# Kernel optimization log

Measured on AMD Instinct MI355X. Metric: run time of the kernel, lower is better.

## Reference

```python
import jax, jax.numpy as jnp
import numpy as np

B, N, D = 16, 128, 128

def setup_inputs() -> dict:
    key = jax.random.key(0)
    ks = jax.random.split(key, 7)
    h = jax.random.normal(ks[0], (B, N, D), dtype=jnp.float32)
    adj = jax.random.randint(ks[1], (B, N, N), 0, 2).astype(jnp.float32)
    e = jax.random.normal(ks[2], (B, N, N, D), dtype=jnp.float32)
    # torch.nn.Linear weights: [out_features, in_features]
    Wm = jax.random.normal(ks[3], (D, 3 * D), dtype=jnp.float32) * (1.0 / np.sqrt(3 * D))
    bm = jax.random.normal(ks[4], (D,), dtype=jnp.float32) * 0.01
    Wu = jax.random.normal(ks[5], (D, 2 * D), dtype=jnp.float32) * (1.0 / np.sqrt(2 * D))
    bu = jax.random.normal(ks[6], (D,), dtype=jnp.float32) * 0.01
    return {"h": h, "adj": adj, "e": e, "Wm": Wm, "bm": bm, "Wu": Wu, "bu": bu}

def reference(h, adj, e, Wm, bm, Wu, bu):
    # Split the message Linear over the concat [h_i, h_j, e] -> three matmuls
    # (same math as cat+Linear, without materializing the [B,N,N,3D] tensor).
    d = h.shape[-1]
    W1, W2, W3 = Wm[:, :d], Wm[:, d:2 * d], Wm[:, 2 * d:]
    hi = jnp.einsum('bnd,kd->bnk', h, W1)            # sender term  [B,N,Dout]
    hj = jnp.einsum('bnd,kd->bnk', h, W2)            # receiver term [B,N,Dout]
    me = jnp.einsum('bijd,kd->bijk', e, W3)          # edge term     [B,N,N,Dout]
    m = hi[:, :, None, :] + hj[:, None, :, :] + me + bm  # [B,N,N,Dout]
    m = m * adj[..., None]                            # mask by adjacency
    m = m.sum(axis=1)                                 # sum over senders i -> [B,N,Dout]
    h_cat = jnp.concatenate([h, m], axis=2)           # [B,N,2D]
    return jnp.einsum('bnd,kd->bnk', h_cat, Wu) + bu  # [B,N,D]
```

## Files before the change

### kernel.cpp

```cpp
#include <hip/hip_runtime.h>
#include <hip/hip_bf16.h>

#define BB 16
#define NN 128
#define DD 128

typedef __attribute__((ext_vector_type(8))) short s8v;
typedef __attribute__((ext_vector_type(4))) float f4v;

__device__ __forceinline__ unsigned short f2bf(float f) {
    __hip_bfloat16 b = __float2bfloat16(f);
    return *reinterpret_cast<unsigned short*>(&b);
}

__global__ __launch_bounds__(256) void prep_kernel(
    const float* __restrict__ h, const float* __restrict__ Wm,
    const float* __restrict__ bm, const float* __restrict__ Wu,
    unsigned short* __restrict__ BT, float* __restrict__ bmWu,
    unsigned short* __restrict__ hbf) {
    const int g = blockIdx.x, t = threadIdx.x;
    if (g < 48) {
        __shared__ float WuB_s[128][129];
        for (int p = 0; p < 64; ++p) {
            const int x = p * 256 + t;
            WuB_s[x & 127][x >> 7] = Wu[(x >> 7) * 256 + 128 + (x & 127)];
        }
        __syncthreads();
        const int m = g >> 4, dc = g & 15;
        const int off   = (m == 0) ? 0   : (m == 1) ? 256 : 128;
        const int rbase = (m == 0) ? 128 : (m == 1) ? 256 : 384;
        const int k = t & 127, dh = t >> 7;
        const int d0 = dc * 8 + dh * 4;
        float a0 = 0, a1 = 0, a2 = 0, a3 = 0;
        for (int kk = 0; kk < 128; ++kk) {
            const float wu = WuB_s[kk][k];
            const float* wmp = Wm + kk * 384 + off + d0;
            a0 += wmp[0] * wu; a1 += wmp[1] * wu;
            a2 += wmp[2] * wu; a3 += wmp[3] * wu;
        }
        unsigned short* bp = BT + (size_t)k * 512 + rbase + d0;
        bp[0] = f2bf(a0); bp[1] = f2bf(a1); bp[2] = f2bf(a2); bp[3] = f2bf(a3);
    } else if (g == 48) {
        for (int p = 0; p < 64; ++p) {
            const int x = p * 256 + t, k = x >> 7, d = x & 127;
            BT[(size_t)k * 512 + d] = f2bf(Wu[k * 256 + d]);
        }
        if (t < 128) {
            float s = 0.f;
            for (int kk = 0; kk < 128; ++kk) s += bm[kk] * Wu[t * 256 + 128 + kk];
            bmWu[t] = s;
        }
    } else {
        const int bi = g - 49;
        const float4* h4 = (const float4*)h;
        uint2* hb2 = (uint2*)hbf;
        for (int p = 0; p < 32; ++p) {
            const int i4 = bi * 8192 + p * 256 + t;
            const float4 v = h4[i4];
            hb2[i4] = make_uint2((unsigned)f2bf(v.x) | ((unsigned)f2bf(v.y) << 16),
                                 (unsigned)f2bf(v.z) | ((unsigned)f2bf(v.w) << 16));
        }
    }
}

__global__ __launch_bounds__(256) void es_kernel(const float* __restrict__ e,
                                                 const float* __restrict__ adj,
                                                 unsigned short* __restrict__ esbf) {
    const int bj = blockIdx.x, t = threadIdx.x;
    const int b = bj >> 7, j = bj & 127;
    __shared__ float adj_s[NN];
    __shared__ float4 red[8][32];
    if (t < NN) adj_s[t] = adj[(size_t)(b * NN + t) * NN + j];
    __syncthreads();
    const int d4 = t & 31, ig = t >> 5;
    const float4* __restrict__ e4 =
        (const float4*)e + ((size_t)(b * NN) * NN + j) * 32 + d4;
    const int i0 = ig * 16;
    float4 acc = make_float4(0.f, 0.f, 0.f, 0.f);
    #pragma unroll
    for (int ii = 0; ii < 16; ++ii) {
        const float a = adj_s[i0 + ii];
        if (a != 0.0f) {
            const float4 v = e4[(size_t)(i0 + ii) * (NN * 32)];
            acc.x += a * v.x; acc.y += a * v.y;
            acc.z += a * v.z; acc.w += a * v.w;
        }
    }
    red[ig][d4] = acc;
    __syncthreads();
    if (t < 32) {
        float4 s = red[0][t];
        #pragma unroll
        for (int r = 1; r < 8; ++r) {
            const float4 v = red[r][t];
            s.x += v.x; s.y += v.y; s.z += v.z; s.w += v.w;
        }
        ((uint2*)esbf)[(size_t)bj * 32 + t] =
            make_uint2((unsigned)f2bf(s.x) | ((unsigned)f2bf(s.y) << 16),
                       (unsigned)f2bf(s.z) | ((unsigned)f2bf(s.w) << 16));
    }
}

__global__ __launch_bounds__(1024) void ah_kernel(
    const float* __restrict__ h, const float* __restrict__ adj,
    unsigned short* __restrict__ AHbf, float* __restrict__ deg) {
    const int blk = blockIdx.x;
    const int b = blk >> 4, jbase = (blk & 15) * 8;
    const int t = threadIdx.x;
    __shared__ float adj_s[8][NN];
    {
        const int i = t >> 3, j2 = t & 7;
        adj_s[j2][i] = adj[(size_t)(b * NN + i) * NN + jbase + j2];
    }
    __syncthreads();
    if (t < 256) {
        const int jj = t >> 5, l = t & 31;
        float s = adj_s[jj][l] + adj_s[jj][l + 32] + adj_s[jj][l + 64] + adj_s[jj][l + 96];
        #pragma unroll
        for (int off = 16; off; off >>= 1) s += __shfl_xor(s, off);
        if (l == 0) deg[b * NN + jbase + jj] = s;
    }
    const int k = t & 127, jl = t >> 7;
    float a0 = 0.f;
    const float* __restrict__ hp = h + (size_t)b * NN * DD + k;
    #pragma unroll 8
    for (int m = 0; m < 32; ++m) {
        const float4 aA = *(const float4*)&adj_s[jl][4 * m];
        const float h0 = hp[(size_t)(4 * m + 0) * DD];
        const float h1 = hp[(size_t)(4 * m + 1) * DD];
        const float h2 = hp[(size_t)(4 * m + 2) * DD];
        const float h3 = hp[(size_t)(4 * m + 3) * DD];
        a0 += aA.x * h0 + aA.y * h1 + aA.z * h2 + aA.w * h3;
    }
    AHbf[(size_t)(b * NN + jbase + jl) * DD + k] = f2bf(a0);
}

__global__ __launch_bounds__(256) void out_kernel(
    const unsigned short* __restrict__ hbf, const unsigned short* __restrict__ AHbf,
    const unsigned short* __restrict__ esbf, const unsigned short* __restrict__ BT,
    const float* __restrict__ deg, const float* __restrict__ bmWu,
    const float* __restrict__ bu, float* __restrict__ out) {
    const int rt = blockIdx.x >> 2, ct = blockIdx.x & 3;
    const int t = threadIdx.x;
    const int l = t & 63, wid = t >> 6, mw = wid >> 1, nw = wid & 1;
    __shared__ unsigned short A_s[32][72], B_s[32][72], B2_s[32][72];
    f4v acc1 = {0.f, 0.f, 0.f, 0.f};
    f4v acc2 = {0.f, 0.f, 0.f, 0.f};
    const int rA = t >> 3, cb = t & 7;
    const int arow = mw * 16 + (l & 15);
    const int brow = nw * 16 + (l & 15);
    const int lg = l >> 4;
    for (int c = 0; c < 6; ++c) {
        __syncthreads();
        const unsigned short* src = (c < 2) ? hbf : (c < 4) ? AHbf : esbf;
        const int col0 = (c & 1) * 64;
        const int rowg = rt * 32 + rA;
        *(s8v*)&A_s[rA][cb * 8] = *(const s8v*)&src[(size_t)rowg * 128 + col0 + cb * 8];
        *(s8v*)&B_s[rA][cb * 8] =
            *(const s8v*)&BT[(size_t)(ct * 32 + rA) * 512 + c * 64 + cb * 8];
        if (c < 2)
            *(s8v*)&B2_s[rA][cb * 8] =
                *(const s8v*)&BT[(size_t)(ct * 32 + rA) * 512 + 384 + c * 64 + cb * 8];
        __syncthreads();
        #pragma unroll
        for (int kit = 0; kit < 2; ++kit) {
            const s8v a  = *(const s8v*)&A_s[arow][kit * 32 + lg * 8];
            const s8v bb = *(const s8v*)&B_s[brow][kit * 32 + lg * 8];
            acc1 = __builtin_amdgcn_mfma_f32_16x16x32_bf16(a, bb, acc1, 0, 0, 0);
            if (c < 2) {
                const s8v b2 = *(const s8v*)&B2_s[brow][kit * 32 + lg * 8];
                acc2 = __builtin_amdgcn_mfma_f32_16x16x32_bf16(a, b2, acc2, 0, 0, 0);
            }
        }
    }
    const int colk = ct * 32 + nw * 16 + (l & 15);
    const float bmv = bmWu[colk], buv = bu[colk];
    #pragma unroll
    for (int r = 0; r < 4; ++r) {
        const int rowg = rt * 32 + mw * 16 + (l >> 4) * 4 + r;
        const float dg = deg[rowg];
        out[(size_t)rowg * 128 + colk] = acc1[r] + dg * acc2[r] + dg * bmv + buv;
    }
}

extern "C" void kernel_launch(void* const* d_in, const int* in_sizes, int n_in,
                              void* d_out, int out_size, void* d_ws, size_t ws_size,
                              hipStream_t stream) {
    const float* h   = (const float*)d_in[0];
    const float* adj = (const float*)d_in[1];
    const float* e   = (const float*)d_in[2];
    const float* Wm  = (const float*)d_in[3];
    const float* bm  = (const float*)d_in[4];
    const float* Wu  = (const float*)d_in[5];
    const float* bu  = (const float*)d_in[6];
    float* out = (float*)d_out;

    float* ws = (float*)d_ws;
    unsigned short* BT   = (unsigned short*)ws;
    float*          bmWu = ws + 32768;
    float*          deg  = ws + 32896;
    unsigned short* hbf  = (unsigned short*)(ws + 34944);
    unsigned short* AHbf = (unsigned short*)(ws + 166016);
    unsigned short* esbf = (unsigned short*)(ws + 297088);

    prep_kernel<<<57, 256, 0, stream>>>(h, Wm, bm, Wu, BT, bmWu, hbf);
    es_kernel<<<BB * NN, 256, 0, stream>>>(e, adj, esbf);
    ah_kernel<<<BB * (NN / 8), 1024, 0, stream>>>(h, adj, AHbf, deg);
    out_kernel<<<256, 256, 0, stream>>>(hbf, AHbf, esbf, BT, deg, bmWu, bu, out);
}
```

Before: 38.08 us.

## Split edge reduction into row-chunked partial sums plus a second reduce pass

```diff
diff --git a/kernel.cpp b/kernel.cpp
--- a/kernel.cpp
+++ b/kernel.cpp
@@ -63,42 +63,65 @@
     }
 }
 
-__global__ __launch_bounds__(256) void es_kernel(const float* __restrict__ e,
-                                                 const float* __restrict__ adj,
-                                                 unsigned short* __restrict__ esbf) {
-    const int bj = blockIdx.x, t = threadIdx.x;
-    const int b = bj >> 7, j = bj & 127;
-    __shared__ float adj_s[NN];
-    __shared__ float4 red[8][32];
-    if (t < NN) adj_s[t] = adj[(size_t)(b * NN + t) * NN + j];
+__global__ __launch_bounds__(256) void es1_kernel(const float* __restrict__ e,
+                                                  const float* __restrict__ adj,
+                                                  float* __restrict__ partial) {
+    const int bid = blockIdx.x;
+    const int b = bid >> 5, ic = (bid >> 1) & 15, jh = bid & 1;
+    const int i0 = ic * 8, j0 = jh * 64;
+    const int t = threadIdx.x;
+
+    __shared__ float adj_s[8][64];
+    #pragma unroll
+    for (int p = 0; p < 2; ++p) {
+        const int x = p * 256 + t;
+        adj_s[x >> 6][x & 63] = adj[(size_t)(b * NN + i0 + (x >> 6)) * NN + j0 + (x & 63)];
+    }
     __syncthreads();
-    const int d4 = t & 31, ig = t >> 5;
-    const float4* __restrict__ e4 =
-        (const float4*)e + ((size_t)(b * NN) * NN + j) * 32 + d4;
-    const int i0 = ig * 16;
-    float4 acc = make_float4(0.f, 0.f, 0.f, 0.f);
-    #pragma unroll
-    for (int ii = 0; ii < 16; ++ii) {
-        const float a = adj_s[i0 + ii];
-        if (a != 0.0f) {
-            const float4 v = e4[(size_t)(i0 + ii) * (NN * 32)];
-            acc.x += a * v.x; acc.y += a * v.y;
-            acc.z += a * v.z; acc.w += a * v.w;
-        }
-    }
-    red[ig][d4] = acc;
-    __syncthreads();
-    if (t < 32) {
-        float4 s = red[0][t];
+
+    const int d4 = t & 31, jg = t >> 5;
+    const float4* __restrict__ e4 = (const float4*)e;
+    f4v acc[8];
+    #pragma unroll
+    for (int q = 0; q < 8; ++q) acc[q] = (f4v){0.f, 0.f, 0.f, 0.f};
+
+    #pragma unroll 2
+    for (int ii = 0; ii < 8; ++ii) {
+        const size_t base = ((size_t)(b * NN + i0 + ii) * NN + j0) * 32 + d4;
         #pragma unroll
-        for (int r = 1; r < 8; ++r) {
-            const float4 v = red[r][t];
-            s.x += v.x; s.y += v.y; s.z += v.z; s.w += v.w;
-        }
-        ((uint2*)esbf)[(size_t)bj * 32 + t] =
-            make_uint2((unsigned)f2bf(s.x) | ((unsigned)f2bf(s.y) << 16),
-                       (unsigned)f2bf(s.z) | ((unsigned)f2bf(s.w) << 16));
-    }
+        for (int q = 0; q < 8; ++q) {
+            const float a = adj_s[ii][jg * 8 + q];
+            if (a != 0.0f) {
+                const float4 v = e4[base + (size_t)(jg * 8 + q) * 32];
+                acc[q].x += a * v.x; acc[q].y += a * v.y;
+                acc[q].z += a * v.z; acc[q].w += a * v.w;
+            }
+        }
+    }
+    float4* __restrict__ p4 = (float4*)partial + (size_t)bid * 2048;
+    #pragma unroll
+    for (int q = 0; q < 8; ++q)
+        p4[(size_t)(jg * 8 + q) * 32 + d4] =
+            make_float4(acc[q].x, acc[q].y, acc[q].z, acc[q].w);
+}
+
+__global__ __launch_bounds__(256) void es2_kernel(const float* __restrict__ partial,
+                                                  unsigned short* __restrict__ esbf) {
+    const int idx = blockIdx.x * 256 + threadIdx.x;
+    const int b = idx >> 12, rem = idx & 4095;
+    const int j = rem >> 5, d4 = rem & 31;
+    const int jh = j >> 6, jrel = j & 63;
+    const float4* __restrict__ p4 = (const float4*)partial;
+    const size_t off = (size_t)jrel * 32 + d4;
+    float4 s = make_float4(0.f, 0.f, 0.f, 0.f);
+    #pragma unroll 4
+    for (int ic = 0; ic < 16; ++ic) {
+        const float4 v = p4[(size_t)(b * 32 + ic * 2 + jh) * 2048 + off];
+        s.x += v.x; s.y += v.y; s.z += v.z; s.w += v.w;
+    }
+    ((uint2*)esbf)[idx] =
+        make_uint2((unsigned)f2bf(s.x) | ((unsigned)f2bf(s.y) << 16),
+                   (unsigned)f2bf(s.z) | ((unsigned)f2bf(s.w) << 16));
 }
 
 __global__ __launch_bounds__(1024) void ah_kernel(
@@ -202,9 +225,11 @@
     unsigned short* hbf  = (unsigned short*)(ws + 34944);
     unsigned short* AHbf = (unsigned short*)(ws + 166016);
     unsigned short* esbf = (unsigned short*)(ws + 297088);
+    float*          partial = ws + 428160;
 
     prep_kernel<<<57, 256, 0, stream>>>(h, Wm, bm, Wu, BT, bmWu, hbf);
-    es_kernel<<<BB * NN, 256, 0, stream>>>(e, adj, esbf);
+    es1_kernel<<<512, 256, 0, stream>>>(e, adj, partial);
+    es2_kernel<<<256, 256, 0, stream>>>(partial, esbf);
     ah_kernel<<<BB * (NN / 8), 1024, 0, stream>>>(h, adj, AHbf, deg);
     out_kernel<<<256, 256, 0, stream>>>(hbf, AHbf, esbf, BT, deg, bmWu, bu, out);
 }
```

New measurement: 88.60 us. 2.33x slower.

## Fuse prep, edge-sum and adjacency-h kernels with ballot-compacted sparse neighbor lists

Applied to the files above, without the earlier changes.

```diff
diff --git a/kernel.cpp b/kernel.cpp
--- a/kernel.cpp
+++ b/kernel.cpp
@@ -13,34 +13,49 @@
     return *reinterpret_cast<unsigned short*>(&b);
 }
 
-__global__ __launch_bounds__(256) void prep_kernel(
-    const float* __restrict__ h, const float* __restrict__ Wm,
+__global__ __launch_bounds__(256, 8) void main_kernel(
+    const float* __restrict__ h, const float* __restrict__ adj,
+    const float* __restrict__ e, const float* __restrict__ Wm,
     const float* __restrict__ bm, const float* __restrict__ Wu,
     unsigned short* __restrict__ BT, float* __restrict__ bmWu,
-    unsigned short* __restrict__ hbf) {
-    const int g = blockIdx.x, t = threadIdx.x;
-    if (g < 48) {
-        __shared__ float WuB_s[128][129];
-        for (int p = 0; p < 64; ++p) {
-            const int x = p * 256 + t;
-            WuB_s[x & 127][x >> 7] = Wu[(x >> 7) * 256 + 128 + (x & 127)];
-        }
-        __syncthreads();
-        const int m = g >> 4, dc = g & 15;
+    unsigned short* __restrict__ hbf, unsigned short* __restrict__ esbf,
+    unsigned short* __restrict__ AHbf, float* __restrict__ deg) {
+    const int bj = blockIdx.x, t = threadIdx.x;
+
+    __shared__ float  sm_big[4096];
+    __shared__ float  sm_adj[NN];
+    __shared__ int    sm_idx[144];
+    __shared__ float  sm_av[144];
+    __shared__ float  sm_ahp[2][NN];
+    __shared__ int    sm_cnt;
+    float4 (*sm_red)[32] = (float4 (*)[32])sm_big;
+
+    if (bj < 48) {
+        float* chunk = sm_big;
+        const int m = bj >> 4, dc = bj & 15;
         const int off   = (m == 0) ? 0   : (m == 1) ? 256 : 128;
         const int rbase = (m == 0) ? 128 : (m == 1) ? 256 : 384;
         const int k = t & 127, dh = t >> 7;
         const int d0 = dc * 8 + dh * 4;
         float a0 = 0, a1 = 0, a2 = 0, a3 = 0;
-        for (int kk = 0; kk < 128; ++kk) {
-            const float wu = WuB_s[kk][k];
-            const float* wmp = Wm + kk * 384 + off + d0;
-            a0 += wmp[0] * wu; a1 += wmp[1] * wu;
-            a2 += wmp[2] * wu; a3 += wmp[3] * wu;
+        for (int c = 0; c < 4; ++c) {
+            for (int x = t; x < 32 * 128; x += 256) {
+                const int kk = x >> 7, kcol = x & 127;
+                chunk[kk * 128 + kcol] = Wu[kcol * 256 + 128 + c * 32 + kk];
+            }
+            __syncthreads();
+            #pragma unroll 8
+            for (int kk = 0; kk < 32; ++kk) {
+                const float wu = chunk[kk * 128 + k];
+                const float* wmp = Wm + (c * 32 + kk) * 384 + off + d0;
+                a0 += wmp[0] * wu; a1 += wmp[1] * wu;
+                a2 += wmp[2] * wu; a3 += wmp[3] * wu;
+            }
+            __syncthreads();
         }
         unsigned short* bp = BT + (size_t)k * 512 + rbase + d0;
         bp[0] = f2bf(a0); bp[1] = f2bf(a1); bp[2] = f2bf(a2); bp[3] = f2bf(a3);
-    } else if (g == 48) {
+    } else if (bj == 48) {
         for (int p = 0; p < 64; ++p) {
             const int x = p * 256 + t, k = x >> 7, d = x & 127;
             BT[(size_t)k * 512 + d] = f2bf(Wu[k * 256 + d]);
@@ -50,8 +65,8 @@
             for (int kk = 0; kk < 128; ++kk) s += bm[kk] * Wu[t * 256 + 128 + kk];
             bmWu[t] = s;
         }
-    } else {
-        const int bi = g - 49;
+    } else if (bj < 57) {
+        const int bi = bj - 49;
         const float4* h4 = (const float4*)h;
         uint2* hb2 = (uint2*)hbf;
         for (int p = 0; p < 32; ++p) {
@@ -61,78 +76,78 @@
                                  (unsigned)f2bf(v.z) | ((unsigned)f2bf(v.w) << 16));
         }
     }
-}
-
-__global__ __launch_bounds__(256) void es_kernel(const float* __restrict__ e,
-                                                 const float* __restrict__ adj,
-                                                 unsigned short* __restrict__ esbf) {
-    const int bj = blockIdx.x, t = threadIdx.x;
+    __syncthreads();
+
     const int b = bj >> 7, j = bj & 127;
-    __shared__ float adj_s[NN];
-    __shared__ float4 red[8][32];
-    if (t < NN) adj_s[t] = adj[(size_t)(b * NN + t) * NN + j];
-    __syncthreads();
-    const int d4 = t & 31, ig = t >> 5;
-    const float4* __restrict__ e4 =
-        (const float4*)e + ((size_t)(b * NN) * NN + j) * 32 + d4;
-    const int i0 = ig * 16;
-    float4 acc = make_float4(0.f, 0.f, 0.f, 0.f);
-    #pragma unroll
-    for (int ii = 0; ii < 16; ++ii) {
-        const float a = adj_s[i0 + ii];
-        if (a != 0.0f) {
-            const float4 v = e4[(size_t)(i0 + ii) * (NN * 32)];
-            acc.x += a * v.x; acc.y += a * v.y;
-            acc.z += a * v.z; acc.w += a * v.w;
-        }
-    }
-    red[ig][d4] = acc;
-    __syncthreads();
+    if (t < NN) sm_adj[t] = adj[(size_t)(b * NN + t) * NN + j];
+    __syncthreads();
+
+    if (t < 64) {
+        const float a0 = sm_adj[t], a1 = sm_adj[t + 64];
+        const unsigned long long m0 = __ballot(a0 != 0.0f);
+        const unsigned long long m1 = __ballot(a1 != 0.0f);
+        const int c0 = __popcll(m0);
+        const unsigned long long below = (t == 0) ? 0ull : ((1ull << t) - 1ull);
+        const int p0 = __popcll(m0 & below);
+        const int p1 = c0 + __popcll(m1 & below);
+        if (a0 != 0.0f) { sm_idx[p0] = t;      sm_av[p0] = a0; }
+        if (a1 != 0.0f) { sm_idx[p1] = t + 64; sm_av[p1] = a1; }
+        const int cnt = c0 + __popcll(m1);
+        const int cntP = (cnt + 15) & ~15;
+        for (int x = cnt + t; x < cntP + 8; x += 64) { sm_idx[x] = 0; sm_av[x] = 0.f; }
+        if (t == 0) sm_cnt = cntP;
+        float s = a0 + a1;
+        #pragma unroll
+        for (int off = 32; off; off >>= 1) s += __shfl_xor(s, off);
+        if (t == 0) deg[bj] = s;
+    }
+    __syncthreads();
+    const int cnt = sm_cnt;
+
+    {
+        const int d4 = t & 31, g = t >> 5;
+        const float4* __restrict__ ep =
+            (const float4*)e + ((size_t)(b * NN) * NN + j) * 32 + d4;
+        f4v acc = {0.f, 0.f, 0.f, 0.f};
+        for (int n = g; n < cnt; n += 16) {
+            const int   iA = sm_idx[n];     const float aA = sm_av[n];
+            const int   iB = sm_idx[n + 8]; const float aB = sm_av[n + 8];
+            const float4 vA = ep[(size_t)iA * (NN * 32)];
+            const float4 vB = ep[(size_t)iB * (NN * 32)];
+            acc.x += aA * vA.x + aB * vB.x;
+            acc.y += aA * vA.y + aB * vB.y;
+            acc.z += aA * vA.z + aB * vB.z;
+            acc.w += aA * vA.w + aB * vB.w;
+        }
+        sm_red[g][d4] = make_float4(acc.x, acc.y, acc.z, acc.w);
+    }
+
+    {
+        const int k = t & 127, ih = t >> 7;
+        float ah = 0.f;
+        const float* __restrict__ hp = h + (size_t)b * NN * DD + k;
+        for (int n = ih; n < cnt; n += 4) {
+            const int   i1 = sm_idx[n];     const float A1 = sm_av[n];
+            const int   i2 = sm_idx[n + 2]; const float A2 = sm_av[n + 2];
+            ah += A1 * hp[(size_t)i1 * DD] + A2 * hp[(size_t)i2 * DD];
+        }
+        sm_ahp[ih][k] = ah;
+    }
+    __syncthreads();
+
     if (t < 32) {
-        float4 s = red[0][t];
+        float4 s = sm_red[0][t];
         #pragma unroll
         for (int r = 1; r < 8; ++r) {
-            const float4 v = red[r][t];
+            const float4 v = sm_red[r][t];
             s.x += v.x; s.y += v.y; s.z += v.z; s.w += v.w;
         }
         ((uint2*)esbf)[(size_t)bj * 32 + t] =
             make_uint2((unsigned)f2bf(s.x) | ((unsigned)f2bf(s.y) << 16),
                        (unsigned)f2bf(s.z) | ((unsigned)f2bf(s.w) << 16));
     }
-}
-
-__global__ __launch_bounds__(1024) void ah_kernel(
-    const float* __restrict__ h, const float* __restrict__ adj,
-    unsigned short* __restrict__ AHbf, float* __restrict__ deg) {
-    const int blk = blockIdx.x;
-    const int b = blk >> 4, jbase = (blk & 15) * 8;
-    const int t = threadIdx.x;
-    __shared__ float adj_s[8][NN];
-    {
-        const int i = t >> 3, j2 = t & 7;
-        adj_s[j2][i] = adj[(size_t)(b * NN + i) * NN + jbase + j2];
-    }
-    __syncthreads();
-    if (t < 256) {
-        const int jj = t >> 5, l = t & 31;
-        float s = adj_s[jj][l] + adj_s[jj][l + 32] + adj_s[jj][l + 64] + adj_s[jj][l + 96];
-        #pragma unroll
-        for (int off = 16; off; off >>= 1) s += __shfl_xor(s, off);
-        if (l == 0) deg[b * NN + jbase + jj] = s;
-    }
-    const int k = t & 127, jl = t >> 7;
-    float a0 = 0.f;
-    const float* __restrict__ hp = h + (size_t)b * NN * DD + k;
-    #pragma unroll 8
-    for (int m = 0; m < 32; ++m) {
-        const float4 aA = *(const float4*)&adj_s[jl][4 * m];
-        const float h0 = hp[(size_t)(4 * m + 0) * DD];
-        const float h1 = hp[(size_t)(4 * m + 1) * DD];
-        const float h2 = hp[(size_t)(4 * m + 2) * DD];
-        const float h3 = hp[(size_t)(4 * m + 3) * DD];
-        a0 += aA.x * h0 + aA.y * h1 + aA.z * h2 + aA.w * h3;
-    }
-    AHbf[(size_t)(b * NN + jbase + jl) * DD + k] = f2bf(a0);
+    if (t < 128)
+        AHbf[(size_t)bj * DD + t] = f2bf(sm_ahp[0][t] + sm_ahp[1][t]);
 }
 
 __global__ __launch_bounds__(256) void out_kernel(
@@ -203,8 +218,7 @@
     unsigned short* AHbf = (unsigned short*)(ws + 166016);
     unsigned short* esbf = (unsigned short*)(ws + 297088);
 
-    prep_kernel<<<57, 256, 0, stream>>>(h, Wm, bm, Wu, BT, bmWu, hbf);
-    es_kernel<<<BB * NN, 256, 0, stream>>>(e, adj, esbf);
-    ah_kernel<<<BB * (NN / 8), 1024, 0, stream>>>(h, adj, AHbf, deg);
+    main_kernel<<<BB * NN, 256, 0, stream>>>(h, adj, e, Wm, bm, Wu,
+                                             BT, bmWu, hbf, esbf, AHbf, deg);
     out_kernel<<<256, 256, 0, stream>>>(hbf, AHbf, esbf, BT, deg, bmWu, bu, out);
 }
```

Result: slower. 57.53 us (+51.1%).

## Merge prep, edge-sum and adjacency-h kernels into one block-dispatched launch

Applied to the files above, without the earlier changes.

```diff
diff --git a/kernel.cpp b/kernel.cpp
--- a/kernel.cpp
+++ b/kernel.cpp
@@ -13,34 +13,115 @@
     return *reinterpret_cast<unsigned short*>(&b);
 }
 
-__global__ __launch_bounds__(256) void prep_kernel(
-    const float* __restrict__ h, const float* __restrict__ Wm,
+__global__ __launch_bounds__(256) void main_kernel(
+    const float* __restrict__ h, const float* __restrict__ adj,
+    const float* __restrict__ e, const float* __restrict__ Wm,
     const float* __restrict__ bm, const float* __restrict__ Wu,
     unsigned short* __restrict__ BT, float* __restrict__ bmWu,
-    unsigned short* __restrict__ hbf) {
-    const int g = blockIdx.x, t = threadIdx.x;
-    if (g < 48) {
-        __shared__ float WuB_s[128][129];
-        for (int p = 0; p < 64; ++p) {
-            const int x = p * 256 + t;
-            WuB_s[x & 127][x >> 7] = Wu[(x >> 7) * 256 + 128 + (x & 127)];
-        }
-        __syncthreads();
+    unsigned short* __restrict__ hbf, unsigned short* __restrict__ esbf,
+    unsigned short* __restrict__ AHbf, float* __restrict__ deg) {
+    const int bid = blockIdx.x, t = threadIdx.x;
+
+    __shared__ float sm_big[4096];
+    __shared__ float sm_adj[NN];
+
+    if (bid < 2048) {
+        const int b = bid >> 7, j = bid & 127;
+        float4 (*red)[32] = (float4 (*)[32])sm_big;
+        if (t < NN) sm_adj[t] = adj[(size_t)(b * NN + t) * NN + j];
+        __syncthreads();
+        const int d4 = t & 31, ig = t >> 5;
+        const float4* __restrict__ e4 =
+            (const float4*)e + ((size_t)(b * NN) * NN + j) * 32 + d4;
+        const int i0 = ig * 16;
+        float4 acc = make_float4(0.f, 0.f, 0.f, 0.f);
+        #pragma unroll
+        for (int ii = 0; ii < 16; ++ii) {
+            const float a = sm_adj[i0 + ii];
+            if (a != 0.0f) {
+                const float4 v = e4[(size_t)(i0 + ii) * (NN * 32)];
+                acc.x += a * v.x; acc.y += a * v.y;
+                acc.z += a * v.z; acc.w += a * v.w;
+            }
+        }
+        red[ig][d4] = acc;
+        __syncthreads();
+        if (t < 32) {
+            float4 s = red[0][t];
+            #pragma unroll
+            for (int r = 1; r < 8; ++r) {
+                const float4 v = red[r][t];
+                s.x += v.x; s.y += v.y; s.z += v.z; s.w += v.w;
+            }
+            ((uint2*)esbf)[(size_t)bid * 32 + t] =
+                make_uint2((unsigned)f2bf(s.x) | ((unsigned)f2bf(s.y) << 16),
+                           (unsigned)f2bf(s.z) | ((unsigned)f2bf(s.w) << 16));
+        }
+    } else if (bid < 2304) {
+        const int b2 = bid - 2048;
+        const int b = b2 >> 4, jbase = (b2 & 15) * 8;
+        float (*adj_s)[NN] = (float (*)[NN])sm_big;
+        for (int x = t; x < 8 * NN; x += 256) {
+            const int i = x >> 3, j2 = x & 7;
+            adj_s[j2][i] = adj[(size_t)(b * NN + i) * NN + jbase + j2];
+        }
+        __syncthreads();
+        {
+            const int jj = t >> 5, l = t & 31;
+            float s = adj_s[jj][l] + adj_s[jj][l + 32] + adj_s[jj][l + 64] + adj_s[jj][l + 96];
+            #pragma unroll
+            for (int off = 16; off; off >>= 1) s += __shfl_xor(s, off);
+            if (l == 0) deg[b * NN + jbase + jj] = s;
+        }
+        const int k = t & 127, jh = t >> 7;
+        float a0 = 0.f, a1 = 0.f, a2 = 0.f, a3 = 0.f;
+        const float* __restrict__ hp = h + (size_t)b * NN * DD + k;
+        #pragma unroll 8
+        for (int m = 0; m < 32; ++m) {
+            const float4 aA = *(const float4*)&adj_s[jh][4 * m];
+            const float4 aB = *(const float4*)&adj_s[jh + 2][4 * m];
+            const float4 aC = *(const float4*)&adj_s[jh + 4][4 * m];
+            const float4 aD = *(const float4*)&adj_s[jh + 6][4 * m];
+            const float h0 = hp[(size_t)(4 * m + 0) * DD];
+            const float h1 = hp[(size_t)(4 * m + 1) * DD];
+            const float h2 = hp[(size_t)(4 * m + 2) * DD];
+            const float h3 = hp[(size_t)(4 * m + 3) * DD];
+            a0 += aA.x * h0 + aA.y * h1 + aA.z * h2 + aA.w * h3;
+            a1 += aB.x * h0 + aB.y * h1 + aB.z * h2 + aB.w * h3;
+            a2 += aC.x * h0 + aC.y * h1 + aC.z * h2 + aC.w * h3;
+            a3 += aD.x * h0 + aD.y * h1 + aD.z * h2 + aD.w * h3;
+        }
+        AHbf[(size_t)(b * NN + jbase + jh) * DD + k]     = f2bf(a0);
+        AHbf[(size_t)(b * NN + jbase + jh + 2) * DD + k] = f2bf(a1);
+        AHbf[(size_t)(b * NN + jbase + jh + 4) * DD + k] = f2bf(a2);
+        AHbf[(size_t)(b * NN + jbase + jh + 6) * DD + k] = f2bf(a3);
+    } else if (bid < 2352) {
+        float* chunk = sm_big;
+        const int g = bid - 2304;
         const int m = g >> 4, dc = g & 15;
         const int off   = (m == 0) ? 0   : (m == 1) ? 256 : 128;
         const int rbase = (m == 0) ? 128 : (m == 1) ? 256 : 384;
         const int k = t & 127, dh = t >> 7;
         const int d0 = dc * 8 + dh * 4;
         float a0 = 0, a1 = 0, a2 = 0, a3 = 0;
-        for (int kk = 0; kk < 128; ++kk) {
-            const float wu = WuB_s[kk][k];
-            const float* wmp = Wm + kk * 384 + off + d0;
-            a0 += wmp[0] * wu; a1 += wmp[1] * wu;
-            a2 += wmp[2] * wu; a3 += wmp[3] * wu;
+        for (int c = 0; c < 4; ++c) {
+            for (int x = t; x < 32 * 128; x += 256) {
+                const int kk = x >> 7, kcol = x & 127;
+                chunk[kk * 128 + kcol] = Wu[kcol * 256 + 128 + c * 32 + kk];
+            }
+            __syncthreads();
+            #pragma unroll 8
+            for (int kk = 0; kk < 32; ++kk) {
+                const float wu = chunk[kk * 128 + k];
+                const float* wmp = Wm + (c * 32 + kk) * 384 + off + d0;
+                a0 += wmp[0] * wu; a1 += wmp[1] * wu;
+                a2 += wmp[2] * wu; a3 += wmp[3] * wu;
+            }
+            __syncthreads();
         }
         unsigned short* bp = BT + (size_t)k * 512 + rbase + d0;
         bp[0] = f2bf(a0); bp[1] = f2bf(a1); bp[2] = f2bf(a2); bp[3] = f2bf(a3);
-    } else if (g == 48) {
+    } else if (bid == 2352) {
         for (int p = 0; p < 64; ++p) {
             const int x = p * 256 + t, k = x >> 7, d = x & 127;
             BT[(size_t)k * 512 + d] = f2bf(Wu[k * 256 + d]);
@@ -51,7 +132,7 @@
             bmWu[t] = s;
         }
     } else {
-        const int bi = g - 49;
+        const int bi = bid - 2353;
         const float4* h4 = (const float4*)h;
         uint2* hb2 = (uint2*)hbf;
         for (int p = 0; p < 32; ++p) {
@@ -61,78 +142,6 @@
                                  (unsigned)f2bf(v.z) | ((unsigned)f2bf(v.w) << 16));
         }
     }
-}
-
-__global__ __launch_bounds__(256) void es_kernel(const float* __restrict__ e,
-                                                 const float* __restrict__ adj,
-                                                 unsigned short* __restrict__ esbf) {
-    const int bj = blockIdx.x, t = threadIdx.x;
-    const int b = bj >> 7, j = bj & 127;
-    __shared__ float adj_s[NN];
-    __shared__ float4 red[8][32];
-    if (t < NN) adj_s[t] = adj[(size_t)(b * NN + t) * NN + j];
-    __syncthreads();
-    const int d4 = t & 31, ig = t >> 5;
-    const float4* __restrict__ e4 =
-        (const float4*)e + ((size_t)(b * NN) * NN + j) * 32 + d4;
-    const int i0 = ig * 16;
-    float4 acc = make_float4(0.f, 0.f, 0.f, 0.f);
-    #pragma unroll
-    for (int ii = 0; ii < 16; ++ii) {
-        const float a = adj_s[i0 + ii];
-        if (a != 0.0f) {
-            const float4 v = e4[(size_t)(i0 + ii) * (NN * 32)];
-            acc.x += a * v.x; acc.y += a * v.y;
-            acc.z += a * v.z; acc.w += a * v.w;
-        }
-    }
-    red[ig][d4] = acc;
-    __syncthreads();
-    if (t < 32) {
-        float4 s = red[0][t];
-        #pragma unroll
-        for (int r = 1; r < 8; ++r) {
-            const float4 v = red[r][t];
-            s.x += v.x; s.y += v.y; s.z += v.z; s.w += v.w;
-        }
-        ((uint2*)esbf)[(size_t)bj * 32 + t] =
-            make_uint2((unsigned)f2bf(s.x) | ((unsigned)f2bf(s.y) << 16),
-                       (unsigned)f2bf(s.z) | ((unsigned)f2bf(s.w) << 16));
-    }
-}
-
-__global__ __launch_bounds__(1024) void ah_kernel(
-    const float* __restrict__ h, const float* __restrict__ adj,
-    unsigned short* __restrict__ AHbf, float* __restrict__ deg) {
-    const int blk = blockIdx.x;
-    const int b = blk >> 4, jbase = (blk & 15) * 8;
-    const int t = threadIdx.x;
-    __shared__ float adj_s[8][NN];
-    {
-        const int i = t >> 3, j2 = t & 7;
-        adj_s[j2][i] = adj[(size_t)(b * NN + i) * NN + jbase + j2];
-    }
-    __syncthreads();
-    if (t < 256) {
-        const int jj = t >> 5, l = t & 31;
-        float s = adj_s[jj][l] + adj_s[jj][l + 32] + adj_s[jj][l + 64] + adj_s[jj][l + 96];
-        #pragma unroll
-        for (int off = 16; off; off >>= 1) s += __shfl_xor(s, off);
-        if (l == 0) deg[b * NN + jbase + jj] = s;
-    }
-    const int k = t & 127, jl = t >> 7;
-    float a0 = 0.f;
-    const float* __restrict__ hp = h + (size_t)b * NN * DD + k;
-    #pragma unroll 8
-    for (int m = 0; m < 32; ++m) {
-        const float4 aA = *(const float4*)&adj_s[jl][4 * m];
-        const float h0 = hp[(size_t)(4 * m + 0) * DD];
-        const float h1 = hp[(size_t)(4 * m + 1) * DD];
-        const float h2 = hp[(size_t)(4 * m + 2) * DD];
-        const float h3 = hp[(size_t)(4 * m + 3) * DD];
-        a0 += aA.x * h0 + aA.y * h1 + aA.z * h2 + aA.w * h3;
-    }
-    AHbf[(size_t)(b * NN + jbase + jl) * DD + k] = f2bf(a0);
 }
 
 __global__ __launch_bounds__(256) void out_kernel(
@@ -203,8 +212,7 @@
     unsigned short* AHbf = (unsigned short*)(ws + 166016);
     unsigned short* esbf = (unsigned short*)(ws + 297088);
 
-    prep_kernel<<<57, 256, 0, stream>>>(h, Wm, bm, Wu, BT, bmWu, hbf);
-    es_kernel<<<BB * NN, 256, 0, stream>>>(e, adj, esbf);
-    ah_kernel<<<BB * (NN / 8), 1024, 0, stream>>>(h, adj, AHbf, deg);
+    main_kernel<<<2361, 256, 0, stream>>>(h, adj, e, Wm, bm, Wu,
+                                          BT, bmWu, hbf, esbf, AHbf, deg);
     out_kernel<<<256, 256, 0, stream>>>(hbf, AHbf, esbf, BT, deg, bmWu, bu, out);
 }
```

Result: no change. 38.69 us (+1.6%).
